# Optimization experiments

Measured on AMD Instinct MI355X. Metric: run time of the kernel, lower is better.

The kernel has to match this reference:

```python
import jax, jax.numpy as jnp
import numpy as np

N = 100_000   # nodes
E = 600_000   # edges
B = 16        # graphs in batch
R = 2         # relations
C = 2         # classes
EPS = 1e-5    # BatchNorm1d eps


def _init(k, shape, fan):
    return jax.random.normal(k, shape, jnp.float32) / np.float32(np.sqrt(fan))


def setup_inputs():
    key = jax.random.key(0)
    ks = jax.random.split(key, 16)
    return {
        "pos": jax.random.normal(ks[0], (N, 3), jnp.float32),
        "edge_index": jax.random.randint(ks[1], (2, E), 0, N),
        "edge_type": jax.random.randint(ks[2], (E,), 0, R),
        "batch": jnp.sort(jax.random.randint(ks[3], (N,), 0, B)),
        # RGCNConv1: in=3, out=64, num_bases=64
        "basis1": _init(ks[4], (64, 3, 64), 3),
        "comp1": _init(ks[5], (R, 64), 64),
        "root1": _init(ks[6], (3, 64), 3),
        "bias1": jnp.zeros((64,), jnp.float32),
        # RGCNConv2: in=64, out=128, num_bases=128
        "basis2": _init(ks[7], (128, 64, 128), 64),
        "comp2": _init(ks[8], (R, 128), 128),
        "root2": _init(ks[9], (64, 128), 64),
        "bias2": jnp.zeros((128,), jnp.float32),
        # lin1 = MLP([128, 1024]): Linear -> ReLU -> BN
        "W_lin1": _init(ks[10], (128, 1024), 128),
        "b_lin1": jnp.zeros((1024,), jnp.float32),
        "g_lin1": jnp.ones((1024,), jnp.float32),
        "be_lin1": jnp.zeros((1024,), jnp.float32),
        # mlp = MLP([1024,512]) -> MLP([512,256]) -> Lin(256, C)
        "W1": _init(ks[11], (1024, 512), 1024),
        "b1": jnp.zeros((512,), jnp.float32),
        "g1": jnp.ones((512,), jnp.float32),
        "be1": jnp.zeros((512,), jnp.float32),
        "W2": _init(ks[12], (512, 256), 512),
        "b2": jnp.zeros((256,), jnp.float32),
        "g2": jnp.ones((256,), jnp.float32),
        "be2": jnp.zeros((256,), jnp.float32),
        "W3": _init(ks[13], (256, C), 256),
        "b3": jnp.zeros((C,), jnp.float32),
    }


def _bn(x, g, b):
    # BatchNorm1d in training mode: batch statistics over the row dim
    m = jnp.mean(x, axis=0)
    v = jnp.var(x, axis=0)
    return (x - m) * jax.lax.rsqrt(v + EPS) * g + b


def _rgcn(x, src, dst, etype, basis, comp, root, bias):
    # Basis decomposition: W[r] = sum_b comp[r, b] * basis[b]
    W = jnp.einsum('rb,bio->rio', comp, basis)
    out = x @ root + bias  # root weight + bias (applied to every node)
    for r in range(R):  # fixed small relation count
        mask = (etype == r).astype(x.dtype)
        # transform then gather: [N,out] -> per-edge message [E,out]
        msg = (x @ W[r])[src] * mask[:, None]
        s = jax.ops.segment_sum(msg, dst, num_segments=N)
        cnt = jax.ops.segment_sum(mask, dst, num_segments=N)
        out = out + s / jnp.maximum(cnt, 1.0)[:, None]  # per-relation mean aggr
    return out


def reference(pos, edge_index, edge_type, batch,
              basis1, comp1, root1, bias1,
              basis2, comp2, root2, bias2,
              W_lin1, b_lin1, g_lin1, be_lin1,
              W1, b1, g1, be1, W2, b2, g2, be2, W3, b3):
    src, dst = edge_index[0], edge_index[1]
    x1 = _rgcn(pos, src, dst, edge_type, basis1, comp1, root1, bias1)
    x2 = _rgcn(x1, src, dst, edge_type, basis2, comp2, root2, bias2)
    h = _bn(jax.nn.relu(x2 @ W_lin1 + b_lin1), g_lin1, be_lin1)  # [N, 1024]
    p = jax.ops.segment_max(h, batch, num_segments=B)            # global max pool
    p = jnp.where(jnp.isfinite(p), p, 0.0)                       # guard empty graphs
    h = _bn(jax.nn.relu(p @ W1 + b1), g1, be1)
    h = _bn(jax.nn.relu(h @ W2 + b2), g2, be2)
    return h @ W3 + b3  # [B, C] logits
```

## Files before the change

kernel.cpp:

```cpp
#include <hip/hip_runtime.h>
#include <stdint.h>
#include <stddef.h>

static const int kN = 100000;
static const int kE = 600000;
static const int kB = 16;
static const int kNB = 200000;

__device__ __forceinline__ float bf2f(unsigned short u){ return __uint_as_float(((unsigned)u) << 16); }
__device__ __forceinline__ unsigned short f2bf(float f){
  unsigned u = __float_as_uint(f);
  u += 0x7FFFu + ((u >> 16) & 1u);
  return (unsigned short)(u >> 16);
}
__device__ __forceinline__ float ldf(const void* p, size_t i, bool isbf){
  return isbf ? bf2f(((const unsigned short*)p)[i]) : ((const float*)p)[i];
}

typedef short bf16x8 __attribute__((ext_vector_type(8)));
typedef _Float16 f16x8 __attribute__((ext_vector_type(8)));
typedef float f32x4 __attribute__((ext_vector_type(4)));
typedef __attribute__((address_space(3))) unsigned int lds_uint;
typedef __attribute__((address_space(1))) const unsigned int gbl_uint;

struct ConvDesc { const void* src; void* dst; int n; };
struct ConvArgs { ConvDesc d[17]; const void* gl; };

__global__ void k_convert(ConvArgs a){
  const ConvDesc cd = a.d[blockIdx.y];
  const bool isbf = (*(const unsigned*)a.gl == 0x3F803F80u);
  int stride = gridDim.x * blockDim.x;
  for (int i = blockIdx.x * blockDim.x + threadIdx.x; i < cd.n; i += stride){
    float f;
    if (isbf) f = bf2f(((const unsigned short*)cd.src)[i]);
    else      f = ((const float*)cd.src)[i];
    ((float*)cd.dst)[i] = f;
  }
}

__global__ void k_wprep(const void* __restrict__ basis1, const void* __restrict__ comp1,
                        float* __restrict__ w1w,
                        const void* __restrict__ basis2, const void* __restrict__ comp2,
                        float* __restrict__ w2f,
                        const void* __restrict__ wf, _Float16* __restrict__ whalf,
                        const void* __restrict__ gl){
  const bool isbf = (*(const unsigned*)gl == 0x3F803F80u);
  int b = blockIdx.x;
  if (b == 0){
    int t = threadIdx.x;
    if (t >= 192) return;
    float a0 = 0.f, a1 = 0.f;
    for (int bb = 0; bb < 64; ++bb){
      float v = ldf(basis1, bb*192 + t, isbf);
      a0 += ldf(comp1, bb, isbf) * v;
      a1 += ldf(comp1, 64 + bb, isbf) * v;
    }
    w1w[t] = a0;
    w1w[192 + t] = a1;
  } else if (b <= 32){
    int id = (b-1)*256 + threadIdx.x;
    if (id >= 8192) return;
    float a0 = 0.f, a1 = 0.f;
    for (int bb = 0; bb < 128; ++bb){
      float v = ldf(basis2, (size_t)bb*8192 + id, isbf);
      a0 += ldf(comp2, bb, isbf) * v;
      a1 += ldf(comp2, 128 + bb, isbf) * v;
    }
    w2f[id]        = a0;
    w2f[8192 + id] = a1;
  } else {
    int id = (b-33)*256 + threadIdx.x;
    float v = ldf(wf, id, isbf);
    _Float16 h = (_Float16)v;
    whalf[id]           = h;
    whalf[131072 + id]  = (_Float16)(v - (float)h);
  }
}

__global__ void k_gprep(const float* __restrict__ root1, const float* __restrict__ bias1,
                        const float* __restrict__ w1w, const void* __restrict__ rt2raw,
                        const float* __restrict__ bias2, const float* __restrict__ w2f,
                        unsigned short* __restrict__ Gh, unsigned short* __restrict__ Gl,
                        float* __restrict__ Cvec, const void* __restrict__ gl){
  const bool isbf = (*(const unsigned*)gl == 0x3F803F80u);
  int id = blockIdx.x*256 + threadIdx.x;
  if (id < 4096){
    int row = id >> 7, c = id & 127;
    float v = 0.f;
    if (row < 21){
      int g = row / 3, i = row - g*3;
      const float* R  = root1 + i*64;
      const float* W0 = w1w + i*64;
      const float* W1 = w1w + 192 + i*64;
      const float* F0 = w2f;
      const float* F1 = w2f + 8192;
      if (g == 0){      for (int j = 0; j < 64; ++j) v += R[j]*ldf(rt2raw, j*128+c, isbf); }
      else if (g == 1){ for (int j = 0; j < 64; ++j) v += W0[j]*ldf(rt2raw, j*128+c, isbf) + R[j]*F0[j*128+c]; }
      else if (g == 2){ for (int j = 0; j < 64; ++j) v += W1[j]*ldf(rt2raw, j*128+c, isbf) + R[j]*F1[j*128+c]; }
      else if (g == 3){ for (int j = 0; j < 64; ++j) v += W0[j]*F0[j*128+c]; }
      else if (g == 4){ for (int j = 0; j < 64; ++j) v += W1[j]*F0[j*128+c]; }
      else if (g == 5){ for (int j = 0; j < 64; ++j) v += W0[j]*F1[j*128+c]; }
      else            { for (int j = 0; j < 64; ++j) v += W1[j]*F1[j*128+c]; }
    }
    unsigned short h = f2bf(v);
    Gh[id] = h;
    Gl[id] = f2bf(v - bf2f(h));
  } else if (id < 4224){
    int c = id - 4096;
    float v = bias2[c];
    for (int j = 0; j < 64; ++j)
      v += bias1[j]*(ldf(rt2raw, j*128+c, isbf) + w2f[j*128+c] + w2f[8192 + j*128+c]);
    Cvec[c] = v;
  }
}

__global__ void k_counti(const int* __restrict__ dst, const int* __restrict__ et,
                         int* __restrict__ cnti){
  int e = blockIdx.x*256 + threadIdx.x;
  if (e >= kE) return;
  atomicAdd(&cnti[dst[e]*2 + et[e]], 1);
}

__global__ void k_scanA(const int* __restrict__ cnti, int* __restrict__ bsum){
  int t = threadIdx.x;
  int base = blockIdx.x*1024 + t*4;
  int s = 0;
  if (base < kNB){ int4 v = *(const int4*)(cnti + base); s = v.x + v.y + v.z + v.w; }
  for (int d = 1; d < 64; d <<= 1) s += __shfl_xor(s, d);
  __shared__ int ws[4];
  if ((t & 63) == 0) ws[t >> 6] = s;
  __syncthreads();
  if (t == 0) bsum[blockIdx.x] = ws[0] + ws[1] + ws[2] + ws[3];
}

__global__ void k_scanC(const int* __restrict__ cnti, const int* __restrict__ bsum,
                        int* __restrict__ offs, int* __restrict__ cur){
  int t = threadIdx.x;
  int base = blockIdx.x*1024 + t*4;
  int4 v = {0,0,0,0};
  if (base < kNB) v = *(const int4*)(cnti + base);
  int s0 = v.x, s01 = v.x + v.y, s012 = s01 + v.z, s = s012 + v.w;
  int lane = t & 63, wv = t >> 6;
  int inc = s;
  for (int d = 1; d < 64; d <<= 1){ int u = __shfl_up(inc, d); if (lane >= d) inc += u; }
  int wexcl = inc - s;
  int vb = (t < blockIdx.x) ? bsum[t] : 0;
  for (int d = 1; d < 64; d <<= 1) vb += __shfl_xor(vb, d);
  __shared__ int wsum[4];
  __shared__ int ws2[4];
  if (lane == 63) wsum[wv] = inc;
  if (lane == 0)  ws2[wv] = vb;
  __syncthreads();
  int bpre_v = ws2[0] + ws2[1] + ws2[2] + ws2[3];
  int woff = 0;
  for (int i = 0; i < wv; ++i) woff += wsum[i];
  int eb = bpre_v + woff + wexcl;
  if (base < kNB){
    int4 o; o.x = eb; o.y = eb + s0; o.z = eb + s01; o.w = eb + s012;
    *(int4*)(offs + base) = o;
    *(int4*)(cur  + base) = o;
  }
}

__global__ void k_scatter(const int* __restrict__ src, const int* __restrict__ dst,
                          const int* __restrict__ et, int* __restrict__ cur,
                          int* __restrict__ esrc){
  int e = blockIdx.x*256 + threadIdx.x;
  if (e >= kE) return;
  int b = dst[e]*2 + et[e];
  int p = atomicAdd(&cur[b], 1);
  esrc[p] = src[e];
}

__global__ void k_agg1(const int* __restrict__ offs, const int* __restrict__ cnti,
                       const int* __restrict__ esrc, const float* __restrict__ pos,
                       float* __restrict__ agg1){
  int b = blockIdx.x*256 + threadIdx.x;
  if (b >= kNB) return;
  int st = offs[b], n = cnti[b];
  float a0 = 0.f, a1 = 0.f, a2 = 0.f;
  if (n > 0){
    int sc_ = esrc[st];
    for (int i = 1; i < n; ++i){
      int sn = esrc[st + i];
      a0 += pos[sc_*3]; a1 += pos[sc_*3+1]; a2 += pos[sc_*3+2];
      sc_ = sn;
    }
    a0 += pos[sc_*3]; a1 += pos[sc_*3+1]; a2 += pos[sc_*3+2];
  }
  float ic = 1.0f / fmaxf((float)n, 1.0f);
  agg1[b*3]   = a0*ic;
  agg1[b*3+1] = a1*ic;
  agg1[b*3+2] = a2*ic;
}

__global__ void k_agg2g(const int* __restrict__ offs, const int* __restrict__ cnti,
                        const int* __restrict__ esrc, const float* __restrict__ agg1,
                        float* __restrict__ agg2p){
  int b = blockIdx.x*256 + threadIdx.x;
  if (b >= kNB) return;
  int st = offs[b], n = cnti[b];
  float a[6] = {0.f,0.f,0.f,0.f,0.f,0.f};
  if (n > 0){
    int sc_ = esrc[st];
    for (int i = 1; i < n; ++i){
      int sn = esrc[st + i];
      #pragma unroll
      for (int j = 0; j < 6; ++j) a[j] += agg1[sc_*6 + j];
      sc_ = sn;
    }
    #pragma unroll
    for (int j = 0; j < 6; ++j) a[j] += agg1[sc_*6 + j];
  }
  float ic = 1.0f / fmaxf((float)n, 1.0f);
  #pragma unroll
  for (int j = 0; j < 6; ++j) agg2p[b*6 + j] = a[j]*ic;
}

__global__ void k_phi(const float* __restrict__ pos, const float* __restrict__ agg1,
                      const float* __restrict__ agg2p, const int* __restrict__ batch,
                      unsigned short* __restrict__ phih, unsigned short* __restrict__ phil,
                      int* __restrict__ gpres){
  int id = blockIdx.x*256 + threadIdx.x;
  int n = id >> 5, c = id & 31;
  float v = 0.f;
  if (c < 3)       v = pos[n*3 + c];
  else if (c < 9)  v = agg1[n*6 + (c-3)];
  else if (c < 21) v = agg2p[(size_t)n*12 + (c-9)];
  unsigned short h = f2bf(v);
  size_t fa = (size_t)(n >> 4)*512 + ((size_t)(c >> 3) << 7) + (n & 15)*8 + (c & 7);
  phih[fa] = h;
  phil[fa] = f2bf(v - bf2f(h));
  if (c == 0) gpres[batch[n]] = 1;
}

__global__ __launch_bounds__(512) void k_xf(const unsigned short* __restrict__ phih,
                 const unsigned short* __restrict__ phil,
                 const unsigned short* __restrict__ Gh, const unsigned short* __restrict__ Gl,
                 const float* __restrict__ Cvec, _Float16* __restrict__ x2f){
  int tid = threadIdx.x, w = tid >> 6, lane = tid & 63;
  int l15 = lane & 15, lg = lane >> 4;
  int cb = w*16;
  bf16x8 bh, bl;
  #pragma unroll
  for (int j = 0; j < 8; ++j){
    int k = lg*8 + j;
    bh[j] = (short)Gh[k*128 + cb + l15];
    bl[j] = (short)Gl[k*128 + cb + l15];
  }
  float cv = Cvec[cb + l15];
  int t0 = blockIdx.x * 10;
  for (int t = t0; t < t0 + 10; ++t){
    size_t pb = (size_t)t*512 + lg*128 + l15*8;
    bf16x8 ah = *(const bf16x8*)(phih + pb);
    bf16x8 al = *(const bf16x8*)(phil + pb);
    f32x4 a0 = {0.f,0.f,0.f,0.f}, a1 = {0.f,0.f,0.f,0.f}, a2 = {0.f,0.f,0.f,0.f};
    a0 = __builtin_amdgcn_mfma_f32_16x16x32_bf16(ah, bh, a0, 0, 0, 0);
    a1 = __builtin_amdgcn_mfma_f32_16x16x32_bf16(al, bh, a1, 0, 0, 0);
    a2 = __builtin_amdgcn_mfma_f32_16x16x32_bf16(ah, bl, a2, 0, 0, 0);
    f32x4 acc = a0 + a1 + a2;
    int c = cb + l15;
    size_t cpart = (size_t)t*2048 + ((size_t)(c >> 3) << 7) + (c & 7);
    #pragma unroll
    for (int j = 0; j < 4; ++j){
      int rl = lg*4 + j;
      x2f[cpart + (rl << 3)] = (_Float16)(acc[j] + cv);
    }
  }
}

__global__ __launch_bounds__(256) void k_gemmF(const _Float16* __restrict__ x2f,
                 const _Float16* __restrict__ whalf,
                 const float* __restrict__ blin, const int* __restrict__ batch,
                 float* __restrict__ colsum, float* __restrict__ colsumsq,
                 float* __restrict__ pool){
  __shared__ __align__(16) _Float16 sA[4][2][2048];
  __shared__ int sBatch[416];
  int b = blockIdx.x;
  int x = b & 7, m = b >> 3;
  int ct = m & 7, j8 = m >> 3;
  int s = x + 8*j8;
  int t0 = s*25 + (s < 50 ? s : 50);
  int nt = (s < 50 ? 26 : 25);
  int t1 = t0 + nt;
  int ns2 = nt >> 1;
  int tail = nt & 1;
  int nstage = ns2 + tail;

  int tid = threadIdx.x, w = tid >> 6, lane = tid & 63;
  int l15 = lane & 15, lg = lane >> 4;
  int cb = ct*128 + w*32;

  for (int i = tid; i < nt*16; i += 256) sBatch[i] = batch[t0*16 + i];

  f16x8 bfrag[2][8];
  #pragma unroll
  for (int cf = 0; cf < 2; ++cf)
    #pragma unroll
    for (int kt = 0; kt < 8; ++kt)
      #pragma unroll
      for (int jj = 0; jj < 8; ++jj){
        int k = (kt < 4 ? kt*32 : (kt-4)*32) + lg*8 + jj;
        size_t plane = (kt < 4) ? 0 : 131072;
        bfrag[cf][kt][jj] = whalf[plane + (size_t)k*1024 + cb + cf*16 + l15];
      }
  float bl[2] = { blin[cb + l15], blin[cb + 16 + l15] };
  __syncthreads();

  auto issueS = [&](int stg){
    int t = t0 + 2*stg;
    if (t > t1 - 1) t = t1 - 1;
    int buf = stg & 3;
    const _Float16* g0 = x2f + (size_t)t*2048;
    const _Float16* g1 = x2f + (size_t)(t+1)*2048;
    int off = w*512 + lane*8;
    __builtin_amdgcn_global_load_lds((gbl_uint*)(g0 + off), (lds_uint*)&sA[buf][0][w*512], 16, 0, 0);
    __builtin_amdgcn_global_load_lds((gbl_uint*)(g1 + off), (lds_uint*)&sA[buf][1][w*512], 16, 0, 0);
  };
  issueS(0); issueS(1); issueS(2);

  float rs[2] = {0.f,0.f}, rq[2] = {0.f,0.f}, rm[2] = {0.f,0.f};
  int curg = sBatch[0];

  auto flushMax = [&](int g){
    #pragma unroll
    for (int cf = 0; cf < 2; ++cf){
      float mx = rm[cf];
      mx = fmaxf(mx, __shfl_xor(mx, 16));
      mx = fmaxf(mx, __shfl_xor(mx, 32));
      if (lg == 0 && mx > 0.f)
        atomicMax((int*)(pool + (size_t)g*1024 + cb + cf*16 + l15), __float_as_int(mx));
    }
  };

  f16x8 af[4];
  auto loadA = [&](int buf, int tile){
    const _Float16* pt = &sA[buf][tile][0];
    #pragma unroll
    for (int kt = 0; kt < 4; ++kt)
      af[kt] = *(const f16x8*)(pt + kt*512 + lg*128 + l15*8);
  };
  auto compute = [&](int rb){
    float v[2][4];
    #pragma unroll
    for (int cf = 0; cf < 2; ++cf){
      f32x4 a0 = {0.f,0.f,0.f,0.f}, a1 = {0.f,0.f,0.f,0.f};
      #pragma unroll
      for (int kt = 0; kt < 4; ++kt)
        a0 = __builtin_amdgcn_mfma_f32_16x16x32_f16(af[kt], bfrag[cf][kt],   a0, 0, 0, 0);
      #pragma unroll
      for (int kt = 0; kt < 4; ++kt)
        a1 = __builtin_amdgcn_mfma_f32_16x16x32_f16(af[kt], bfrag[cf][4+kt], a1, 0, 0, 0);
      f32x4 acc = a0 + a1;
      #pragma unroll
      for (int jj = 0; jj < 4; ++jj){
        float xv = fmaxf(acc[jj] + bl[cf], 0.f);
        v[cf][jj] = xv;
        rs[cf] += xv;
        rq[cf] += xv*xv;
      }
    }
    int g0 = sBatch[rb], g15 = sBatch[rb + 15];
    if (g0 == g15){
      if (g0 != curg){ flushMax(curg); rm[0] = rm[1] = 0.f; curg = g0; }
      #pragma unroll
      for (int cf = 0; cf < 2; ++cf)
        rm[cf] = fmaxf(rm[cf], fmaxf(fmaxf(v[cf][0], v[cf][1]), fmaxf(v[cf][2], v[cf][3])));
    } else {
      flushMax(curg); rm[0] = rm[1] = 0.f;
      #pragma unroll
      for (int jj = 0; jj < 4; ++jj){
        int g = sBatch[rb + lg*4 + jj];
        #pragma unroll
        for (int cf = 0; cf < 2; ++cf)
          if (v[cf][jj] > 0.f)
            atomicMax((int*)(pool + (size_t)g*1024 + cb + cf*16 + l15), __float_as_int(v[cf][jj]));
      }
      curg = g15;
    }
  };

  for (int st = 0; st < nstage; ++st){
    int buf = st & 3;
    asm volatile("s_waitcnt vmcnt(4)" ::: "memory");
    __builtin_amdgcn_sched_barrier(0);
    __builtin_amdgcn_s_barrier();
    issueS(st + 3);
    loadA(buf, 0);
    asm volatile("s_waitcnt lgkmcnt(0)" ::: "memory");
    __builtin_amdgcn_sched_barrier(0);
    compute(st*32);
    if (st < ns2){
      loadA(buf, 1);
      asm volatile("s_waitcnt lgkmcnt(0)" ::: "memory");
      __builtin_amdgcn_sched_barrier(0);
      compute(st*32 + 16);
    }
  }
  flushMax(curg);
  #pragma unroll
  for (int cf = 0; cf < 2; ++cf){
    rs[cf] += __shfl_xor(rs[cf], 16); rs[cf] += __shfl_xor(rs[cf], 32);
    rq[cf] += __shfl_xor(rq[cf], 16); rq[cf] += __shfl_xor(rq[cf], 32);
  }
  if (lg == 0){
    #pragma unroll
    for (int cf = 0; cf < 2; ++cf){
      atomicAdd(&colsum[cb + cf*16 + l15],  rs[cf]);
      atomicAdd(&colsumsq[cb + cf*16 + l15], rq[cf]);
    }
  }
}

__global__ __launch_bounds__(256) void k_denseP1f(const float* __restrict__ colsum,
                 const float* __restrict__ colsumsq, const float* __restrict__ pool,
                 const int* __restrict__ gpres, const float* __restrict__ gl,
                 const float* __restrict__ bel, const float* __restrict__ W,
                 float* __restrict__ zpart){
  int k0 = blockIdx.y * 64;
  __shared__ float Xs[16*64];
  for (int idx = threadIdx.x; idx < 1024; idx += 256){
    int r = idx >> 6, kk = idx & 63;
    int c = k0 + kk;
    float m = colsum[c] * (1.0f/kN);
    float var = colsumsq[c] * (1.0f/kN) - m*m;
    float sc = rsqrtf(var + 1e-5f) * gl[c];
    Xs[idx] = gpres[r] ? (pool[(size_t)r*1024 + c] - m)*sc + bel[c] : 0.0f;
  }
  __syncthreads();
  int c = blockIdx.x*256 + threadIdx.x;
  float acc[16];
  #pragma unroll
  for (int g = 0; g < 16; ++g) acc[g] = 0.f;
  for (int kk = 0; kk < 64; ++kk){
    float wv = W[(size_t)(k0 + kk)*512 + c];
    #pragma unroll
    for (int g = 0; g < 16; ++g) acc[g] += Xs[g*64 + kk] * wv;
  }
  float* zp = zpart + ((size_t)blockIdx.y*16)*512 + c;
  #pragma unroll
  for (int g = 0; g < 16; ++g) zp[(size_t)g*512] = acc[g];
}

__global__ __launch_bounds__(256) void k_denseP(const float* __restrict__ X,
                 const float* __restrict__ W, float* __restrict__ zpart,
                 int K, int C){
  const int KS = 16;
  int Kc = K / KS;
  int k0 = blockIdx.y * Kc;
  __shared__ float Xs[16*64];
  for (int idx = threadIdx.x; idx < 16*Kc; idx += 256){
    int r = idx / Kc, kk = idx - r*Kc;
    Xs[idx] = X[r*K + k0 + kk];
  }
  __syncthreads();
  int c = blockIdx.x*256 + threadIdx.x;
  float acc[16];
  #pragma unroll
  for (int g = 0; g < 16; ++g) acc[g] = 0.f;
  for (int kk = 0; kk < Kc; ++kk){
    float wv = W[(size_t)(k0 + kk)*C + c];
    #pragma unroll
    for (int g = 0; g < 16; ++g) acc[g] += Xs[g*Kc + kk] * wv;
  }
  float* zp = zpart + ((size_t)blockIdx.y*16)*C + c;
  #pragma unroll
  for (int g = 0; g < 16; ++g) zp[(size_t)g*C] = acc[g];
}

__global__ void k_gbnf(const float* __restrict__ zpart, const float* __restrict__ bias,
                       const float* __restrict__ gg, const float* __restrict__ bb,
                       float* __restrict__ z, int C){
  const int KS = 16;
  int o = blockIdx.x*256 + threadIdx.x;
  if (o >= C) return;
  float vv[16], s = 0.f, q = 0.f;
  #pragma unroll
  for (int r = 0; r < 16; ++r){
    float v = bias[o];
    for (int ks = 0; ks < KS; ++ks) v += zpart[((size_t)ks*16 + r)*C + o];
    v = fmaxf(v, 0.f);
    vv[r] = v; s += v; q += v*v;
  }
  float m = s * (1.0f/16.0f);
  float var = q * (1.0f/16.0f) - m*m;
  float sc = rsqrtf(var + 1e-5f) * gg[o];
  float be = bb[o];
  #pragma unroll
  for (int r = 0; r < 16; ++r) z[(size_t)r*C + o] = (vv[r] - m)*sc + be;
}

__global__ void k_g3(const float* __restrict__ z2, const float* __restrict__ W3,
                     const float* __restrict__ b3, const void* __restrict__ glraw,
                     void* __restrict__ dout){
  int t = threadIdx.x;
  if (t >= 32) return;
  int g = t >> 1, j = t & 1;
  float s = b3[j];
  for (int k = 0; k < 256; ++k) s += z2[g*256 + k] * W3[k*2 + j];
  bool isbf = (*(const unsigned*)glraw == 0x3F803F80u);
  if (isbf) ((unsigned short*)dout)[t] = f2bf(s);
  else      ((float*)dout)[t] = s;
}

extern "C" void kernel_launch(void* const* d_in, const int* in_sizes, int n_in,
                              void* d_out, int out_size, void* d_ws, size_t ws_size,
                              hipStream_t stream){
  (void)in_sizes; (void)n_in; (void)out_size; (void)ws_size;
  static const int convSizes[17] = {300000,192,64,128,1024,1024,1024,524288,
                                    512,512,512,131072,256,256,256,512,2};
  static const int convSrc[17]   = {0,6,7,11,13,14,15,16,17,18,19,20,21,22,23,24,25};
  size_t coff[18]; coff[0] = 0;
  for (int i = 0; i < 17; ++i) coff[i+1] = coff[i] + (size_t)convSizes[i];

  char* wsb = (char*)d_ws;
  float* convF = (float*)wsb;
  size_t cur_ = (coff[17]*4 + 255) & ~(size_t)255;
  auto take = [&](size_t bytes)->char*{
    char* p = wsb + cur_; cur_ = (cur_ + bytes + 255) & ~(size_t)255; return p;
  };
  float* w1w             = (float*)take(384*4);
  float* w2f             = (float*)take((size_t)16384*4);
  _Float16* whalf        = (_Float16*)take((size_t)262144*2);
  unsigned short* Gh     = (unsigned short*)take(4096*2);
  unsigned short* Gl     = (unsigned short*)take(4096*2);
  float* Cvec            = (float*)take(128*4);
  size_t zstart = cur_;
  int*   cnti     = (int*)take((size_t)kNB*4);
  float* colsum   = (float*)take(1024*4);
  float* colsumsq = (float*)take(1024*4);
  float* pool     = (float*)take((size_t)kB*1024*4);
  int*   gpres    = (int*)take(kB*4);
  size_t zbytes = cur_ - zstart;
  int*   offs  = (int*)take((size_t)kNB*4);
  int*   curC  = (int*)take((size_t)kNB*4);
  int*   bsum  = (int*)take(256*4);
  int*   esrc  = (int*)take((size_t)kE*4);
  float* agg1  = (float*)take((size_t)kNB*3*4);
  float* agg2p = (float*)take((size_t)kNB*6*4);
  unsigned short* phih  = (unsigned short*)take((size_t)kN*32*2);
  unsigned short* phil  = (unsigned short*)take((size_t)kN*32*2);
  _Float16* x2f         = (_Float16*)take(((size_t)kN*128 + 4096)*2);
  float* zp1 = (float*)take((size_t)16*16*512*4);
  float* zp2 = (float*)take((size_t)16*16*256*4);
  float* z1  = (float*)take((size_t)kB*512*4);
  float* z2  = (float*)take((size_t)kB*256*4);

  const int* ei    = (const int*)d_in[1];
  const int* src   = ei;
  const int* dst   = ei + kE;
  const int* et    = (const int*)d_in[2];
  const int* batch = (const int*)d_in[3];

  ConvArgs ca;
  for (int i = 0; i < 17; ++i)
    ca.d[i] = { d_in[convSrc[i]], convF + coff[i], convSizes[i] };
  ca.gl = d_in[14];

  hipMemsetAsync(wsb + zstart, 0, zbytes, stream);
  k_convert<<<dim3(128,17), 256, 0, stream>>>(ca);
  k_wprep<<<545, 256, 0, stream>>>(d_in[4], d_in[5], w1w,
                                   d_in[8], d_in[9], w2f,
                                   d_in[12], whalf, d_in[14]);
  k_gprep<<<17, 256, 0, stream>>>(convF+coff[1], convF+coff[2], w1w, d_in[10],
                                  convF+coff[3], w2f, Gh, Gl, Cvec, d_in[14]);
  k_counti<<<(kE+255)/256, 256, 0, stream>>>(dst, et, cnti);
  k_scanA<<<196, 256, 0, stream>>>(cnti, bsum);
  k_scanC<<<196, 256, 0, stream>>>(cnti, bsum, offs, curC);
  k_scatter<<<(kE+255)/256, 256, 0, stream>>>(src, dst, et, curC, esrc);
  k_agg1<<<(kNB+255)/256, 256, 0, stream>>>(offs, cnti, esrc, convF+coff[0], agg1);
  k_agg2g<<<(kNB+255)/256, 256, 0, stream>>>(offs, cnti, esrc, agg1, agg2p);
  k_phi<<<kN*32/256, 256, 0, stream>>>(convF+coff[0], agg1, agg2p, batch,
                                       phih, phil, gpres);
  k_xf<<<625, 512, 0, stream>>>(phih, phil, Gh, Gl, Cvec, x2f);
  k_gemmF<<<1984, 256, 0, stream>>>(x2f, whalf, convF+coff[4], batch,
                                    colsum, colsumsq, pool);
  k_denseP1f<<<dim3(2,16), 256, 0, stream>>>(colsum, colsumsq, pool, gpres,
                                             convF+coff[5], convF+coff[6],
                                             convF+coff[7], zp1);
  k_gbnf<<<2, 256, 0, stream>>>(zp1, convF+coff[8], convF+coff[9], convF+coff[10], z1, 512);
  k_denseP<<<dim3(1,16), 256, 0, stream>>>(z1, convF+coff[11], zp2, 512, 256);
  k_gbnf<<<1, 256, 0, stream>>>(zp2, convF+coff[12], convF+coff[13], convF+coff[14], z2, 256);
  k_g3<<<1, 64, 0, stream>>>(z2, convF+coff[15], convF+coff[16], d_in[14], d_out);
}
```

Baseline: 251.1 us.

## Fold the RGCN feature transform into lin1 weights and drop the x2 intermediate

Since x2 is a linear function of the 21-wide feature vector phi, the change precomputes GW = G·W_lin1 (21x1024, split into bf16 hi/lo) and a fused bias Cw, then has the main GEMM consume phi directly. This removes the k_xf kernel, the N×128 fp16 x2 buffer write and read, and shrinks the per-tile K from 128 to 32. The cost is a small extra prep kernel and three bf16 MFMAs per fragment for split precision. Reassociating the two matmuls also changes rounding behaviour.

```diff
diff --git a/kernel.cpp b/kernel.cpp
--- a/kernel.cpp
+++ b/kernel.cpp
@@ -18,7 +18,6 @@
 }
 
 typedef short bf16x8 __attribute__((ext_vector_type(8)));
-typedef _Float16 f16x8 __attribute__((ext_vector_type(8)));
 typedef float f32x4 __attribute__((ext_vector_type(4)));
 typedef __attribute__((address_space(3))) unsigned int lds_uint;
 typedef __attribute__((address_space(1))) const unsigned int gbl_uint;
@@ -41,9 +40,7 @@
 __global__ void k_wprep(const void* __restrict__ basis1, const void* __restrict__ comp1,
                         float* __restrict__ w1w,
                         const void* __restrict__ basis2, const void* __restrict__ comp2,
-                        float* __restrict__ w2f,
-                        const void* __restrict__ wf, _Float16* __restrict__ whalf,
-                        const void* __restrict__ gl){
+                        float* __restrict__ w2f, const void* __restrict__ gl){
   const bool isbf = (*(const unsigned*)gl == 0x3F803F80u);
   int b = blockIdx.x;
   if (b == 0){
@@ -57,7 +54,7 @@
     }
     w1w[t] = a0;
     w1w[192 + t] = a1;
-  } else if (b <= 32){
+  } else {
     int id = (b-1)*256 + threadIdx.x;
     if (id >= 8192) return;
     float a0 = 0.f, a1 = 0.f;
@@ -68,20 +65,14 @@
     }
     w2f[id]        = a0;
     w2f[8192 + id] = a1;
-  } else {
-    int id = (b-33)*256 + threadIdx.x;
-    float v = ldf(wf, id, isbf);
-    _Float16 h = (_Float16)v;
-    whalf[id]           = h;
-    whalf[131072 + id]  = (_Float16)(v - (float)h);
   }
 }
 
 __global__ void k_gprep(const float* __restrict__ root1, const float* __restrict__ bias1,
                         const float* __restrict__ w1w, const void* __restrict__ rt2raw,
                         const float* __restrict__ bias2, const float* __restrict__ w2f,
-                        unsigned short* __restrict__ Gh, unsigned short* __restrict__ Gl,
-                        float* __restrict__ Cvec, const void* __restrict__ gl){
+                        float* __restrict__ Gf, float* __restrict__ Cvec,
+                        const void* __restrict__ gl){
   const bool isbf = (*(const unsigned*)gl == 0x3F803F80u);
   int id = blockIdx.x*256 + threadIdx.x;
   if (id < 4096){
@@ -102,15 +93,35 @@
       else if (g == 5){ for (int j = 0; j < 64; ++j) v += W0[j]*F1[j*128+c]; }
       else            { for (int j = 0; j < 64; ++j) v += W1[j]*F1[j*128+c]; }
     }
-    unsigned short h = f2bf(v);
-    Gh[id] = h;
-    Gl[id] = f2bf(v - bf2f(h));
+    Gf[id] = v;
   } else if (id < 4224){
     int c = id - 4096;
     float v = bias2[c];
     for (int j = 0; j < 64; ++j)
       v += bias1[j]*(ldf(rt2raw, j*128+c, isbf) + w2f[j*128+c] + w2f[8192 + j*128+c]);
     Cvec[c] = v;
+  }
+}
+
+__global__ void k_gw(const float* __restrict__ Gf, const float* __restrict__ Cvec,
+                     const void* __restrict__ wfraw, const float* __restrict__ blin,
+                     unsigned short* __restrict__ GWh, unsigned short* __restrict__ GWl,
+                     float* __restrict__ Cw, const void* __restrict__ gl){
+  const bool isbf = (*(const unsigned*)gl == 0x3F803F80u);
+  int id = blockIdx.x*256 + threadIdx.x;
+  if (id < 32768){
+    int k = id >> 10, c = id & 1023;
+    float v = 0.f;
+    if (k < 21)
+      for (int j = 0; j < 128; ++j) v += Gf[k*128 + j] * ldf(wfraw, (size_t)j*1024 + c, isbf);
+    unsigned short h = f2bf(v);
+    GWh[id] = h;
+    GWl[id] = f2bf(v - bf2f(h));
+  } else if (id < 33792){
+    int c = id - 32768;
+    float v = blin[c];
+    for (int j = 0; j < 128; ++j) v += Cvec[j] * ldf(wfraw, (size_t)j*1024 + c, isbf);
+    Cw[c] = v;
   }
 }
 
@@ -234,47 +245,13 @@
   if (c == 0) gpres[batch[n]] = 1;
 }
 
-__global__ __launch_bounds__(512) void k_xf(const unsigned short* __restrict__ phih,
+__global__ __launch_bounds__(256) void k_gemmF(const unsigned short* __restrict__ phih,
                  const unsigned short* __restrict__ phil,
-                 const unsigned short* __restrict__ Gh, const unsigned short* __restrict__ Gl,
-                 const float* __restrict__ Cvec, _Float16* __restrict__ x2f){
-  int tid = threadIdx.x, w = tid >> 6, lane = tid & 63;
-  int l15 = lane & 15, lg = lane >> 4;
-  int cb = w*16;
-  bf16x8 bh, bl;
-  #pragma unroll
-  for (int j = 0; j < 8; ++j){
-    int k = lg*8 + j;
-    bh[j] = (short)Gh[k*128 + cb + l15];
-    bl[j] = (short)Gl[k*128 + cb + l15];
-  }
-  float cv = Cvec[cb + l15];
-  int t0 = blockIdx.x * 10;
-  for (int t = t0; t < t0 + 10; ++t){
-    size_t pb = (size_t)t*512 + lg*128 + l15*8;
-    bf16x8 ah = *(const bf16x8*)(phih + pb);
-    bf16x8 al = *(const bf16x8*)(phil + pb);
-    f32x4 a0 = {0.f,0.f,0.f,0.f}, a1 = {0.f,0.f,0.f,0.f}, a2 = {0.f,0.f,0.f,0.f};
-    a0 = __builtin_amdgcn_mfma_f32_16x16x32_bf16(ah, bh, a0, 0, 0, 0);
-    a1 = __builtin_amdgcn_mfma_f32_16x16x32_bf16(al, bh, a1, 0, 0, 0);
-    a2 = __builtin_amdgcn_mfma_f32_16x16x32_bf16(ah, bl, a2, 0, 0, 0);
-    f32x4 acc = a0 + a1 + a2;
-    int c = cb + l15;
-    size_t cpart = (size_t)t*2048 + ((size_t)(c >> 3) << 7) + (c & 7);
-    #pragma unroll
-    for (int j = 0; j < 4; ++j){
-      int rl = lg*4 + j;
-      x2f[cpart + (rl << 3)] = (_Float16)(acc[j] + cv);
-    }
-  }
-}
-
-__global__ __launch_bounds__(256) void k_gemmF(const _Float16* __restrict__ x2f,
-                 const _Float16* __restrict__ whalf,
-                 const float* __restrict__ blin, const int* __restrict__ batch,
+                 const unsigned short* __restrict__ GWh, const unsigned short* __restrict__ GWl,
+                 const float* __restrict__ Cw, const int* __restrict__ batch,
                  float* __restrict__ colsum, float* __restrict__ colsumsq,
                  float* __restrict__ pool){
-  __shared__ __align__(16) _Float16 sA[4][2][2048];
+  __shared__ __align__(16) unsigned short sA[4][4][512];
   __shared__ int sBatch[416];
   int b = blockIdx.x;
   int x = b & 7, m = b >> 3;
@@ -293,29 +270,26 @@
 
   for (int i = tid; i < nt*16; i += 256) sBatch[i] = batch[t0*16 + i];
 
-  f16x8 bfrag[2][8];
+  bf16x8 gw[2][2];
   #pragma unroll
   for (int cf = 0; cf < 2; ++cf)
     #pragma unroll
-    for (int kt = 0; kt < 8; ++kt)
-      #pragma unroll
-      for (int jj = 0; jj < 8; ++jj){
-        int k = (kt < 4 ? kt*32 : (kt-4)*32) + lg*8 + jj;
-        size_t plane = (kt < 4) ? 0 : 131072;
-        bfrag[cf][kt][jj] = whalf[plane + (size_t)k*1024 + cb + cf*16 + l15];
-      }
-  float bl[2] = { blin[cb + l15], blin[cb + 16 + l15] };
+    for (int j = 0; j < 8; ++j){
+      int k = lg*8 + j;
+      int c = cb + cf*16 + l15;
+      gw[cf][0][j] = (short)GWh[(size_t)k*1024 + c];
+      gw[cf][1][j] = (short)GWl[(size_t)k*1024 + c];
+    }
+  float bl[2] = { Cw[cb + l15], Cw[cb + 16 + l15] };
   __syncthreads();
 
   auto issueS = [&](int stg){
-    int t = t0 + 2*stg;
+    int t = t0 + 2*stg + (w >> 1);
     if (t > t1 - 1) t = t1 - 1;
     int buf = stg & 3;
-    const _Float16* g0 = x2f + (size_t)t*2048;
-    const _Float16* g1 = x2f + (size_t)(t+1)*2048;
-    int off = w*512 + lane*8;
-    __builtin_amdgcn_global_load_lds((gbl_uint*)(g0 + off), (lds_uint*)&sA[buf][0][w*512], 16, 0, 0);
-    __builtin_amdgcn_global_load_lds((gbl_uint*)(g1 + off), (lds_uint*)&sA[buf][1][w*512], 16, 0, 0);
+    const unsigned short* g = (w & 1) ? phil : phih;
+    __builtin_amdgcn_global_load_lds((gbl_uint*)(g + (size_t)t*512 + lane*8),
+                                     (lds_uint*)&sA[buf][w][lane*8], 16, 0, 0);
   };
   issueS(0); issueS(1); issueS(2);
 
@@ -333,25 +307,20 @@
     }
   };
 
-  f16x8 af[4];
+  bf16x8 ah, al;
   auto loadA = [&](int buf, int tile){
-    const _Float16* pt = &sA[buf][tile][0];
-    #pragma unroll
-    for (int kt = 0; kt < 4; ++kt)
-      af[kt] = *(const f16x8*)(pt + kt*512 + lg*128 + l15*8);
+    ah = *(const bf16x8*)(&sA[buf][tile*2    ][lg*128 + l15*8]);
+    al = *(const bf16x8*)(&sA[buf][tile*2 + 1][lg*128 + l15*8]);
   };
   auto compute = [&](int rb){
     float v[2][4];
     #pragma unroll
     for (int cf = 0; cf < 2; ++cf){
-      f32x4 a0 = {0.f,0.f,0.f,0.f}, a1 = {0.f,0.f,0.f,0.f};
-      #pragma unroll
-      for (int kt = 0; kt < 4; ++kt)
-        a0 = __builtin_amdgcn_mfma_f32_16x16x32_f16(af[kt], bfrag[cf][kt],   a0, 0, 0, 0);
-      #pragma unroll
-      for (int kt = 0; kt < 4; ++kt)
-        a1 = __builtin_amdgcn_mfma_f32_16x16x32_f16(af[kt], bfrag[cf][4+kt], a1, 0, 0, 0);
-      f32x4 acc = a0 + a1;
+      f32x4 a0 = {0.f,0.f,0.f,0.f}, a1 = {0.f,0.f,0.f,0.f}, a2 = {0.f,0.f,0.f,0.f};
+      a0 = __builtin_amdgcn_mfma_f32_16x16x32_bf16(ah, gw[cf][0], a0, 0, 0, 0);
+      a1 = __builtin_amdgcn_mfma_f32_16x16x32_bf16(al, gw[cf][0], a1, 0, 0, 0);
+      a2 = __builtin_amdgcn_mfma_f32_16x16x32_bf16(ah, gw[cf][1], a2, 0, 0, 0);
+      f32x4 acc = a0 + a1 + a2;
       #pragma unroll
       for (int jj = 0; jj < 4; ++jj){
         float xv = fmaxf(acc[jj] + bl[cf], 0.f);
@@ -382,7 +351,7 @@
 
   for (int st = 0; st < nstage; ++st){
     int buf = st & 3;
-    asm volatile("s_waitcnt vmcnt(4)" ::: "memory");
+    asm volatile("s_waitcnt vmcnt(2)" ::: "memory");
     __builtin_amdgcn_sched_barrier(0);
     __builtin_amdgcn_s_barrier();
     issueS(st + 3);
@@ -521,10 +490,11 @@
   };
   float* w1w             = (float*)take(384*4);
   float* w2f             = (float*)take((size_t)16384*4);
-  _Float16* whalf        = (_Float16*)take((size_t)262144*2);
-  unsigned short* Gh     = (unsigned short*)take(4096*2);
-  unsigned short* Gl     = (unsigned short*)take(4096*2);
+  float* Gf              = (float*)take(4096*4);
   float* Cvec            = (float*)take(128*4);
+  unsigned short* GWh    = (unsigned short*)take((size_t)32768*2);
+  unsigned short* GWl    = (unsigned short*)take((size_t)32768*2);
+  float* Cw              = (float*)take(1024*4);
   size_t zstart = cur_;
   int*   cnti     = (int*)take((size_t)kNB*4);
   float* colsum   = (float*)take(1024*4);
@@ -538,9 +508,8 @@
   int*   esrc  = (int*)take((size_t)kE*4);
   float* agg1  = (float*)take((size_t)kNB*3*4);
   float* agg2p = (float*)take((size_t)kNB*6*4);
-  unsigned short* phih  = (unsigned short*)take((size_t)kN*32*2);
-  unsigned short* phil  = (unsigned short*)take((size_t)kN*32*2);
-  _Float16* x2f         = (_Float16*)take(((size_t)kN*128 + 4096)*2);
+  unsigned short* phih  = (unsigned short*)take(((size_t)kN*32 + 1024)*2);
+  unsigned short* phil  = (unsigned short*)take(((size_t)kN*32 + 1024)*2);
   float* zp1 = (float*)take((size_t)16*16*512*4);
   float* zp2 = (float*)take((size_t)16*16*256*4);
   float* z1  = (float*)take((size_t)kB*512*4);
@@ -559,11 +528,10 @@
 
   hipMemsetAsync(wsb + zstart, 0, zbytes, stream);
   k_convert<<<dim3(128,17), 256, 0, stream>>>(ca);
-  k_wprep<<<545, 256, 0, stream>>>(d_in[4], d_in[5], w1w,
-                                   d_in[8], d_in[9], w2f,
-                                   d_in[12], whalf, d_in[14]);
+  k_wprep<<<33, 256, 0, stream>>>(d_in[4], d_in[5], w1w, d_in[8], d_in[9], w2f, d_in[14]);
   k_gprep<<<17, 256, 0, stream>>>(convF+coff[1], convF+coff[2], w1w, d_in[10],
-                                  convF+coff[3], w2f, Gh, Gl, Cvec, d_in[14]);
+                                  convF+coff[3], w2f, Gf, Cvec, d_in[14]);
+  k_gw<<<132, 256, 0, stream>>>(Gf, Cvec, d_in[12], convF+coff[4], GWh, GWl, Cw, d_in[14]);
   k_counti<<<(kE+255)/256, 256, 0, stream>>>(dst, et, cnti);
   k_scanA<<<196, 256, 0, stream>>>(cnti, bsum);
   k_scanC<<<196, 256, 0, stream>>>(cnti, bsum, offs, curC);
@@ -572,8 +540,7 @@
   k_agg2g<<<(kNB+255)/256, 256, 0, stream>>>(offs, cnti, esrc, agg1, agg2p);
   k_phi<<<kN*32/256, 256, 0, stream>>>(convF+coff[0], agg1, agg2p, batch,
                                        phih, phil, gpres);
-  k_xf<<<625, 512, 0, stream>>>(phih, phil, Gh, Gl, Cvec, x2f);
-  k_gemmF<<<1984, 256, 0, stream>>>(x2f, whalf, convF+coff[4], batch,
+  k_gemmF<<<1984, 256, 0, stream>>>(phih, phil, GWh, GWl, Cw, batch,
                                     colsum, colsumsq, pool);
   k_denseP1f<<<dim3(2,16), 256, 0, stream>>>(colsum, colsumsq, pool, gpres,
                                              convF+coff[5], convF+coff[6],
```

Result: faster. 229.1 us (median of 2 runs) (-8.7%).
